# Optimization experiments

Measured on AMD Instinct MI355X. Metric: run time of the kernel, lower is better.

Reference implementation:

```python
import jax, jax.numpy as jnp
import numpy as np

# FUME epipolar image translation: for each output pixel p2=(x2,y2) the fundamental
# matrix F maps it to a line l = F @ [x2*d, y2*d, 1] in the input view (full-res
# coordinates; d = per-batch downsampling factor). The output value is the line
# integral of the input image along that epipolar line, computed by stepping one
# pixel at a time along the dominant axis with bilinear (1-D linear) interpolation
# across the other axis; out-of-bounds samples contribute zero.

def _translate(img, F, d):
    B, C, H, W = img.shape
    dt = img.dtype
    yy, xx = jnp.meshgrid(jnp.arange(H, dtype=dt), jnp.arange(W, dtype=dt), indexing='ij')
    db = d[:, None, None].astype(dt)                          # (B,1,1)
    px, py = xx[None] * db, yy[None] * db                     # (B,H,W) full-res coords
    a = F[0, 0] * px + F[0, 1] * py + F[0, 2]                 # line coeffs l = F @ [x,y,1]
    b = F[1, 0] * px + F[1, 1] * py + F[1, 2]
    c = F[2, 0] * px + F[2, 1] * py + F[2, 2]
    horiz = jnp.abs(b) >= jnp.abs(a)                          # dominant axis per pixel

    db4 = db[..., None]                                       # (B,1,1,1)
    # horizontal traversal: step over columns s, solve a*(s*d) + b*(y*d) + c = 0
    s = jnp.arange(W, dtype=dt)
    denom_h = jnp.where(horiz, b, jnp.ones((), dt))[..., None] * db4
    yline = -(a[..., None] * (s * db4) + c[..., None]) / denom_h    # (B,H,W,W)
    # vertical traversal: step over rows t, solve for x
    t = jnp.arange(H, dtype=dt)
    denom_v = jnp.where(horiz, jnp.ones((), dt), a)[..., None] * db4
    xline = -(b[..., None] * (t * db4) + c[..., None]) / denom_v    # (B,H,W,H)

    def sample_one(imgb, y, x):
        # imgb: (C,H,W); y: (H,W,W) row coord per column step; x: (H,W,H) col coord per row step
        y0 = jnp.floor(y)
        wy = y - y0
        y0i = jnp.clip(y0.astype(jnp.int32), 0, H - 1)
        y1i = jnp.clip(y0i + 1, 0, H - 1)
        cols = jnp.arange(W)
        vh = (1 - wy)[None] * imgb[:, y0i, cols] + wy[None] * imgb[:, y1i, cols]  # (C,H,W,W)
        vh = jnp.where(((y >= 0) & (y <= H - 1))[None], vh, jnp.zeros((), imgb.dtype)).sum(-1)

        x0 = jnp.floor(x)
        wx = x - x0
        x0i = jnp.clip(x0.astype(jnp.int32), 0, W - 1)
        x1i = jnp.clip(x0i + 1, 0, W - 1)
        rows = jnp.arange(H)
        vv = (1 - wx)[None] * imgb[:, rows, x0i] + wx[None] * imgb[:, rows, x1i]  # (C,H,W,H)
        vv = jnp.where(((x >= 0) & (x <= W - 1))[None], vv, jnp.zeros((), imgb.dtype)).sum(-1)
        return vh, vv

    vh, vv = jax.vmap(sample_one)(img, yline, xline)          # each (B,C,H,W)
    return jnp.where(horiz[:, None], vh, vv)


def setup_inputs() -> dict:
    key = jax.random.key(0)
    k1, k2, k3 = jax.random.split(key, 3)
    B, C, H, W = 4, 4, 128, 128
    view1 = jax.random.normal(k1, (B, C, H, W), jnp.float32)
    F21 = jax.random.normal(k2, (3, 3), jnp.float32)
    F12 = jax.random.normal(k3, (3, 3), jnp.float32)
    downsampled_factor = jnp.ones((B,), jnp.float32)
    return {"view1": view1, "F21": F21, "F12": F12, "downsampled_factor": downsampled_factor}


def reference(view1, F21, F12, downsampled_factor):
    # forward uses F21 only; F12 is kept for the backward pass in the original module
    return _translate(view1, F21, downsampled_factor)
```

## Files before the change

### kernel.cpp

```cpp
#include <hip/hip_runtime.h>


#define CC 4
#define HH 128
#define WW 128
#define LDK 144
#define CUBE (128 * LDK)

typedef _Float16 h2 __attribute__((ext_vector_type(2)));

__global__ void __launch_bounds__(256) fume_stage(
        const float* __restrict__ img, float4* __restrict__ ws) {
    __shared__ float tile[4][17][17];
    int x0 = blockIdx.x * 16, y0 = blockIdx.y * 16, b = blockIdx.z;
    int tx = threadIdx.x, ty = threadIdx.y;
    int id = ty * 16 + tx;
    const float* src = img + (size_t)b * CC * HH * WW;

    #pragma unroll
    for (int ch = 0; ch < 4; ++ch) {
        #pragma unroll
        for (int e = 0; e < 2; ++e) {
            int idx = id + e * 256;
            if (idx < 289) {
                int i = idx / 17, j = idx % 17;
                int r = min(y0 + i, HH - 1);
                int c = min(x0 + j, WW - 1);
                tile[ch][i][j] = src[(ch * HH + r) * WW + c];
            }
        }
    }
    __syncthreads();

    float4* base_h = ws + (size_t)b * (2 * CUBE);
    float4* base_v = base_h + CUBE;

    {
        h2 p0 = { (_Float16)tile[0][ty][tx], (_Float16)tile[0][ty][tx + 1] };
        h2 p1 = { (_Float16)tile[1][ty][tx], (_Float16)tile[1][ty][tx + 1] };
        h2 p2 = { (_Float16)tile[2][ty][tx], (_Float16)tile[2][ty][tx + 1] };
        h2 p3 = { (_Float16)tile[3][ty][tx], (_Float16)tile[3][ty][tx + 1] };
        float4 e = make_float4(__builtin_bit_cast(float, p0),
                               __builtin_bit_cast(float, p1),
                               __builtin_bit_cast(float, p2),
                               __builtin_bit_cast(float, p3));
        base_v[(y0 + ty) * LDK + (x0 + tx)] = e;
    }
    {
        h2 p0 = { (_Float16)tile[0][tx][ty], (_Float16)tile[0][tx + 1][ty] };
        h2 p1 = { (_Float16)tile[1][tx][ty], (_Float16)tile[1][tx + 1][ty] };
        h2 p2 = { (_Float16)tile[2][tx][ty], (_Float16)tile[2][tx + 1][ty] };
        h2 p3 = { (_Float16)tile[3][tx][ty], (_Float16)tile[3][tx + 1][ty] };
        float4 e = make_float4(__builtin_bit_cast(float, p0),
                               __builtin_bit_cast(float, p1),
                               __builtin_bit_cast(float, p2),
                               __builtin_bit_cast(float, p3));
        base_h[(x0 + ty) * LDK + (y0 + tx)] = e;
    }
}

__global__ void __launch_bounds__(512) fume_kernel(
        const float4* __restrict__ cubes,
        const float* __restrict__ F,
        const float* __restrict__ dsf,
        float* __restrict__ out) {
    int tx  = threadIdx.x;
    int seg = threadIdx.y;
    int x = blockIdx.x * 64 + tx;
    int y = blockIdx.y;
    int b = blockIdx.z;

    float d = dsf[b];
    float F00 = F[0], F01 = F[1], F02 = F[2];
    float F10 = F[3], F11 = F[4], F12 = F[5];
    float F20 = F[6], F21 = F[7], F22 = F[8];

    float px = __fmul_rn((float)x, d);
    float py = __fmul_rn((float)y, d);
    float av = __fadd_rn(__fadd_rn(__fmul_rn(F00, px), __fmul_rn(F01, py)), F02);
    float bv = __fadd_rn(__fadd_rn(__fmul_rn(F10, px), __fmul_rn(F11, py)), F12);
    float cv = __fadd_rn(__fadd_rn(__fmul_rn(F20, px), __fmul_rn(F21, py)), F22);

    bool horiz  = fabsf(bv) >= fabsf(av);
    float ncoef = horiz ? av : bv;
    float den   = __fmul_rn(horiz ? bv : av, d);
    float nrec  = -__fdiv_rn(1.0f, den);

    const float4* P = cubes + (size_t)b * (2 * CUBE) + (horiz ? 0 : CUBE);

    float A  = __fmul_rn(__fmul_rn(ncoef, d), nrec);
    float Bc = __fmul_rn(cv, nrec);
    int lkmin, lkmax;
    if (fabsf(A) > 1e-20f) {
        float inv = 1.0f / A;
        float k1 = (0.0f   - Bc) * inv;
        float k2 = (127.0f - Bc) * inv;
        float lo = fmaxf(fminf(k1, k2) - 2.0f, 0.0f);
        float hi = fminf(fmaxf(k1, k2) + 2.0f, 127.0f);
        if (lo > hi || !(lo == lo)) { lkmin = 1; lkmax = 0; }
        else { lkmin = (int)lo; lkmax = (int)hi; }
    } else {
        bool full = (Bc >= 0.0f) && (Bc <= 127.0f);
        lkmin = full ? 0 : 1;
        lkmax = full ? 127 : 0;
    }

    float a0 = 0.f, a1 = 0.f, a2 = 0.f, a3 = 0.f;
    int len = lkmax - lkmin + 1;
    int cnt = (len + 7) >> 3;
    int ks  = lkmin + seg * cnt;
    int ke  = min(ks + cnt - 1, lkmax);
    #pragma unroll 8
    for (int k = ks; k <= ke; ++k) {
        float m  = __fmul_rn((float)k, d);
        float q  = __fadd_rn(__fmul_rn(ncoef, m), cv);
        float u  = __fmul_rn(q, nrec);
        bool ok  = (u >= 0.f) && (u <= 127.f);
        int i0   = (int)floorf(u);
        i0 = max(0, min(i0, 126));
        float w  = __fsub_rn(u, (float)i0);
        h2 wp = __builtin_bit_cast(h2,
                    __builtin_amdgcn_cvt_pkrtz(__fsub_rn(1.f, w), w));
        wp = ok ? wp : (h2){(_Float16)0.f, (_Float16)0.f};
        float4 e = P[k * LDK + i0];
        a0 = __builtin_amdgcn_fdot2(wp, __builtin_bit_cast(h2, e.x), a0, false);
        a1 = __builtin_amdgcn_fdot2(wp, __builtin_bit_cast(h2, e.y), a1, false);
        a2 = __builtin_amdgcn_fdot2(wp, __builtin_bit_cast(h2, e.z), a2, false);
        a3 = __builtin_amdgcn_fdot2(wp, __builtin_bit_cast(h2, e.w), a3, false);
    }

    __shared__ float part[8][4][64];
    part[seg][0][tx] = a0;
    part[seg][1][tx] = a1;
    part[seg][2][tx] = a2;
    part[seg][3][tx] = a3;
    __syncthreads();

    if (seg < 4) {
        int ch = seg;
        float s = part[0][ch][tx];
        #pragma unroll
        for (int t = 1; t < 8; ++t) s = __fadd_rn(s, part[t][ch][tx]);
        out[(((size_t)b * CC + ch) * HH + y) * WW + x] = s;
    }
}

extern "C" void kernel_launch(void* const* d_in, const int* in_sizes, int n_in,
                              void* d_out, int out_size, void* d_ws, size_t ws_size,
                              hipStream_t stream) {
    const float* view1 = (const float*)d_in[0];
    const float* F21   = (const float*)d_in[1];
    const float* dsf   = (const float*)d_in[3];

    const int B = in_sizes[3];

    dim3 stb(16, 16, 1);
    dim3 stg(WW / 16, HH / 16, B);
    fume_stage<<<stg, stb, 0, stream>>>(view1, (float4*)d_ws);

    dim3 ftb(64, 8, 1);
    dim3 ftg(WW / 64, HH, B);
    fume_kernel<<<ftg, ftb, 0, stream>>>((const float4*)d_ws, F21, dsf,
                                         (float*)d_out);
}
```

Baseline: 68.34 us.

## Assign one wavefront per output pixel with lanes over steps and shuffle reduction

The staged fp16 cubes are transposed so the step index k is contiguous, and each 64-lane wavefront now handles a single output pixel, with lanes covering consecutive steps. Partial sums are combined with a wavefront xor-shuffle reduction, which removes the shared-memory partial buffer and the block barrier. The goal is coalesced gathers across lanes, since neighbouring steps touch adjacent k columns, and balanced work per lane. The cost is more blocks and more per-pixel line setup, which is now repeated by all 64 lanes, and lanes go idle for pixels whose valid step range is short.

```diff
diff --git a/kernel.cpp b/kernel.cpp
--- a/kernel.cpp
+++ b/kernel.cpp
@@ -4,7 +4,7 @@
 #define CC 4
 #define HH 128
 #define WW 128
-#define LDK 144
+#define LDK 128
 #define CUBE (128 * LDK)
 
 typedef _Float16 h2 __attribute__((ext_vector_type(2)));
@@ -36,26 +36,26 @@
     float4* base_v = base_h + CUBE;
 
     {
-        h2 p0 = { (_Float16)tile[0][ty][tx], (_Float16)tile[0][ty][tx + 1] };
-        h2 p1 = { (_Float16)tile[1][ty][tx], (_Float16)tile[1][ty][tx + 1] };
-        h2 p2 = { (_Float16)tile[2][ty][tx], (_Float16)tile[2][ty][tx + 1] };
-        h2 p3 = { (_Float16)tile[3][ty][tx], (_Float16)tile[3][ty][tx + 1] };
+        h2 p0 = { (_Float16)tile[0][ty][tx], (_Float16)tile[0][ty + 1][tx] };
+        h2 p1 = { (_Float16)tile[1][ty][tx], (_Float16)tile[1][ty + 1][tx] };
+        h2 p2 = { (_Float16)tile[2][ty][tx], (_Float16)tile[2][ty + 1][tx] };
+        h2 p3 = { (_Float16)tile[3][ty][tx], (_Float16)tile[3][ty + 1][tx] };
         float4 e = make_float4(__builtin_bit_cast(float, p0),
                                __builtin_bit_cast(float, p1),
                                __builtin_bit_cast(float, p2),
                                __builtin_bit_cast(float, p3));
-        base_v[(y0 + ty) * LDK + (x0 + tx)] = e;
+        base_h[(y0 + ty) * LDK + (x0 + tx)] = e;
     }
     {
-        h2 p0 = { (_Float16)tile[0][tx][ty], (_Float16)tile[0][tx + 1][ty] };
-        h2 p1 = { (_Float16)tile[1][tx][ty], (_Float16)tile[1][tx + 1][ty] };
-        h2 p2 = { (_Float16)tile[2][tx][ty], (_Float16)tile[2][tx + 1][ty] };
-        h2 p3 = { (_Float16)tile[3][tx][ty], (_Float16)tile[3][tx + 1][ty] };
+        h2 p0 = { (_Float16)tile[0][tx][ty], (_Float16)tile[0][tx][ty + 1] };
+        h2 p1 = { (_Float16)tile[1][tx][ty], (_Float16)tile[1][tx][ty + 1] };
+        h2 p2 = { (_Float16)tile[2][tx][ty], (_Float16)tile[2][tx][ty + 1] };
+        h2 p3 = { (_Float16)tile[3][tx][ty], (_Float16)tile[3][tx][ty + 1] };
         float4 e = make_float4(__builtin_bit_cast(float, p0),
                                __builtin_bit_cast(float, p1),
                                __builtin_bit_cast(float, p2),
                                __builtin_bit_cast(float, p3));
-        base_h[(x0 + ty) * LDK + (y0 + tx)] = e;
+        base_v[(x0 + ty) * LDK + (y0 + tx)] = e;
     }
 }
 
@@ -64,9 +64,9 @@
         const float* __restrict__ F,
         const float* __restrict__ dsf,
         float* __restrict__ out) {
-    int tx  = threadIdx.x;
-    int seg = threadIdx.y;
-    int x = blockIdx.x * 64 + tx;
+    int j = threadIdx.x;
+    int w = threadIdx.y;
+    int x = blockIdx.x * 8 + w;
     int y = blockIdx.y;
     int b = blockIdx.z;
 
@@ -106,42 +106,39 @@
     }
 
     float a0 = 0.f, a1 = 0.f, a2 = 0.f, a3 = 0.f;
-    int len = lkmax - lkmin + 1;
-    int cnt = (len + 7) >> 3;
-    int ks  = lkmin + seg * cnt;
-    int ke  = min(ks + cnt - 1, lkmax);
-    #pragma unroll 8
-    for (int k = ks; k <= ke; ++k) {
-        float m  = __fmul_rn((float)k, d);
-        float q  = __fadd_rn(__fmul_rn(ncoef, m), cv);
-        float u  = __fmul_rn(q, nrec);
-        bool ok  = (u >= 0.f) && (u <= 127.f);
-        int i0   = (int)floorf(u);
-        i0 = max(0, min(i0, 126));
-        float w  = __fsub_rn(u, (float)i0);
-        h2 wp = __builtin_bit_cast(h2,
-                    __builtin_amdgcn_cvt_pkrtz(__fsub_rn(1.f, w), w));
-        wp = ok ? wp : (h2){(_Float16)0.f, (_Float16)0.f};
-        float4 e = P[k * LDK + i0];
-        a0 = __builtin_amdgcn_fdot2(wp, __builtin_bit_cast(h2, e.x), a0, false);
-        a1 = __builtin_amdgcn_fdot2(wp, __builtin_bit_cast(h2, e.y), a1, false);
-        a2 = __builtin_amdgcn_fdot2(wp, __builtin_bit_cast(h2, e.z), a2, false);
-        a3 = __builtin_amdgcn_fdot2(wp, __builtin_bit_cast(h2, e.w), a3, false);
+    #pragma unroll
+    for (int t = 0; t < 2; ++t) {
+        int k = lkmin + (t << 6) + j;
+        if (k <= lkmax) {
+            float m  = __fmul_rn((float)k, d);
+            float q  = __fadd_rn(__fmul_rn(ncoef, m), cv);
+            float u  = __fmul_rn(q, nrec);
+            bool ok  = (u >= 0.f) && (u <= 127.f);
+            int i0   = (int)floorf(u);
+            i0 = max(0, min(i0, 126));
+            float wq = __fsub_rn(u, (float)i0);
+            h2 wp = __builtin_bit_cast(h2,
+                        __builtin_amdgcn_cvt_pkrtz(__fsub_rn(1.f, wq), wq));
+            wp = ok ? wp : (h2){(_Float16)0.f, (_Float16)0.f};
+            float4 e = P[i0 * LDK + k];
+            a0 = __builtin_amdgcn_fdot2(wp, __builtin_bit_cast(h2, e.x), a0, false);
+            a1 = __builtin_amdgcn_fdot2(wp, __builtin_bit_cast(h2, e.y), a1, false);
+            a2 = __builtin_amdgcn_fdot2(wp, __builtin_bit_cast(h2, e.z), a2, false);
+            a3 = __builtin_amdgcn_fdot2(wp, __builtin_bit_cast(h2, e.w), a3, false);
+        }
     }
 
-    __shared__ float part[8][4][64];
-    part[seg][0][tx] = a0;
-    part[seg][1][tx] = a1;
-    part[seg][2][tx] = a2;
-    part[seg][3][tx] = a3;
-    __syncthreads();
+    #pragma unroll
+    for (int mlt = 32; mlt >= 1; mlt >>= 1) {
+        a0 = __fadd_rn(a0, __shfl_xor(a0, mlt));
+        a1 = __fadd_rn(a1, __shfl_xor(a1, mlt));
+        a2 = __fadd_rn(a2, __shfl_xor(a2, mlt));
+        a3 = __fadd_rn(a3, __shfl_xor(a3, mlt));
+    }
 
-    if (seg < 4) {
-        int ch = seg;
-        float s = part[0][ch][tx];
-        #pragma unroll
-        for (int t = 1; t < 8; ++t) s = __fadd_rn(s, part[t][ch][tx]);
-        out[(((size_t)b * CC + ch) * HH + y) * WW + x] = s;
+    if (j < 4) {
+        float v = (j == 0) ? a0 : (j == 1) ? a1 : (j == 2) ? a2 : a3;
+        out[(((size_t)b * CC + j) * HH + y) * WW + x] = v;
     }
 }
 
@@ -159,7 +156,7 @@
     fume_stage<<<stg, stb, 0, stream>>>(view1, (float4*)d_ws);
 
     dim3 ftb(64, 8, 1);
-    dim3 ftg(WW / 64, HH, B);
+    dim3 ftg(WW / 8, HH, B);
     fume_kernel<<<ftg, ftb, 0, stream>>>((const float4*)d_ws, F21, dsf,
                                          (float*)d_out);
 }
```

Measured after the change: 79.32 us. 1.16x slower.

## Transpose sample cube layout and build it without shared-memory tiling

Applied to the files above, without the earlier changes.

The staged fp16 pair cube is now stored as [interpolation index][step index] with an unpadded 128 stride instead of [step][index] with a 144 stride. The main kernel's gather indexing is changed to match. The staging kernel drops the 16x16 shared-memory tile and transpose: each thread reads its two neighbouring source samples straight from global memory, with a grid split by direction. This removes the LDS round trip and a barrier in staging. In exchange, the column-direction reads become strided, and the main kernel's per-thread gathers now differ mostly by row (2 KB stride), which may coalesce worse.

```diff
diff --git a/kernel.cpp b/kernel.cpp
--- a/kernel.cpp
+++ b/kernel.cpp
@@ -4,59 +4,37 @@
 #define CC 4
 #define HH 128
 #define WW 128
-#define LDK 144
+#define LDK 128
 #define CUBE (128 * LDK)
 
 typedef _Float16 h2 __attribute__((ext_vector_type(2)));
 
-__global__ void __launch_bounds__(256) fume_stage(
+__global__ void __launch_bounds__(128) fume_stage(
         const float* __restrict__ img, float4* __restrict__ ws) {
-    __shared__ float tile[4][17][17];
-    int x0 = blockIdx.x * 16, y0 = blockIdx.y * 16, b = blockIdx.z;
-    int tx = threadIdx.x, ty = threadIdx.y;
-    int id = ty * 16 + tx;
+    int t   = threadIdx.x;
+    int u   = blockIdx.x;
+    int dir = blockIdx.y;
+    int b   = blockIdx.z;
     const float* src = img + (size_t)b * CC * HH * WW;
+    float4* base = ws + (size_t)b * (2 * CUBE) + (dir ? CUBE : 0);
+    int u1 = min(u + 1, HH - 1);
 
-    #pragma unroll
-    for (int ch = 0; ch < 4; ++ch) {
-        #pragma unroll
-        for (int e = 0; e < 2; ++e) {
-            int idx = id + e * 256;
-            if (idx < 289) {
-                int i = idx / 17, j = idx % 17;
-                int r = min(y0 + i, HH - 1);
-                int c = min(x0 + j, WW - 1);
-                tile[ch][i][j] = src[(ch * HH + r) * WW + c];
-            }
-        }
+    h2 p0, p1, p2, p3;
+    if (dir == 0) {
+        p0 = (h2){ (_Float16)src[(0 * HH + u) * WW + t], (_Float16)src[(0 * HH + u1) * WW + t] };
+        p1 = (h2){ (_Float16)src[(1 * HH + u) * WW + t], (_Float16)src[(1 * HH + u1) * WW + t] };
+        p2 = (h2){ (_Float16)src[(2 * HH + u) * WW + t], (_Float16)src[(2 * HH + u1) * WW + t] };
+        p3 = (h2){ (_Float16)src[(3 * HH + u) * WW + t], (_Float16)src[(3 * HH + u1) * WW + t] };
+    } else {
+        p0 = (h2){ (_Float16)src[(0 * HH + t) * WW + u], (_Float16)src[(0 * HH + t) * WW + u1] };
+        p1 = (h2){ (_Float16)src[(1 * HH + t) * WW + u], (_Float16)src[(1 * HH + t) * WW + u1] };
+        p2 = (h2){ (_Float16)src[(2 * HH + t) * WW + u], (_Float16)src[(2 * HH + t) * WW + u1] };
+        p3 = (h2){ (_Float16)src[(3 * HH + t) * WW + u], (_Float16)src[(3 * HH + t) * WW + u1] };
     }
-    __syncthreads();
-
-    float4* base_h = ws + (size_t)b * (2 * CUBE);
-    float4* base_v = base_h + CUBE;
-
-    {
-        h2 p0 = { (_Float16)tile[0][ty][tx], (_Float16)tile[0][ty][tx + 1] };
-        h2 p1 = { (_Float16)tile[1][ty][tx], (_Float16)tile[1][ty][tx + 1] };
-        h2 p2 = { (_Float16)tile[2][ty][tx], (_Float16)tile[2][ty][tx + 1] };
-        h2 p3 = { (_Float16)tile[3][ty][tx], (_Float16)tile[3][ty][tx + 1] };
-        float4 e = make_float4(__builtin_bit_cast(float, p0),
-                               __builtin_bit_cast(float, p1),
-                               __builtin_bit_cast(float, p2),
-                               __builtin_bit_cast(float, p3));
-        base_v[(y0 + ty) * LDK + (x0 + tx)] = e;
-    }
-    {
-        h2 p0 = { (_Float16)tile[0][tx][ty], (_Float16)tile[0][tx + 1][ty] };
-        h2 p1 = { (_Float16)tile[1][tx][ty], (_Float16)tile[1][tx + 1][ty] };
-        h2 p2 = { (_Float16)tile[2][tx][ty], (_Float16)tile[2][tx + 1][ty] };
-        h2 p3 = { (_Float16)tile[3][tx][ty], (_Float16)tile[3][tx + 1][ty] };
-        float4 e = make_float4(__builtin_bit_cast(float, p0),
-                               __builtin_bit_cast(float, p1),
-                               __builtin_bit_cast(float, p2),
-                               __builtin_bit_cast(float, p3));
-        base_h[(x0 + ty) * LDK + (y0 + tx)] = e;
-    }
+    base[u * LDK + t] = make_float4(__builtin_bit_cast(float, p0),
+                                    __builtin_bit_cast(float, p1),
+                                    __builtin_bit_cast(float, p2),
+                                    __builtin_bit_cast(float, p3));
 }
 
 __global__ void __launch_bounds__(512) fume_kernel(
@@ -122,7 +100,7 @@
         h2 wp = __builtin_bit_cast(h2,
                     __builtin_amdgcn_cvt_pkrtz(__fsub_rn(1.f, w), w));
         wp = ok ? wp : (h2){(_Float16)0.f, (_Float16)0.f};
-        float4 e = P[k * LDK + i0];
+        float4 e = P[i0 * LDK + k];
         a0 = __builtin_amdgcn_fdot2(wp, __builtin_bit_cast(h2, e.x), a0, false);
         a1 = __builtin_amdgcn_fdot2(wp, __builtin_bit_cast(h2, e.y), a1, false);
         a2 = __builtin_amdgcn_fdot2(wp, __builtin_bit_cast(h2, e.z), a2, false);
@@ -154,8 +132,8 @@
 
     const int B = in_sizes[3];
 
-    dim3 stb(16, 16, 1);
-    dim3 stg(WW / 16, HH / 16, B);
+    dim3 stb(128, 1, 1);
+    dim3 stg(HH, 2, B);
     fume_stage<<<stg, stb, 0, stream>>>(view1, (float4*)d_ws);
 
     dim3 ftb(64, 8, 1);
```

Result: no change. 69.69 us (+2.0%).
